# Performance work log

Hardware: AMD Instinct MI355X
Metric: run time of the kernel (lower is better)

Reference implementation:

```python
import jax, jax.numpy as jnp
import numpy as np

B, N, M = 8, 1024, 1024
DIM2 = 1280          # config.dim * 2
KIN = 1344           # esm_dim + cell_line_dim
H, DK = 8, 64        # heads, attn_dim_key
SCALE = DK ** -0.5


def setup_inputs() -> dict:
    key = jax.random.key(0)
    ks = jax.random.split(key, 7)
    rna_reps = jax.random.normal(ks[0], (B, N, DIM2), dtype=jnp.float32)
    protein_reps = jax.random.normal(ks[1], (B, M, KIN), dtype=jnp.float32)
    # learned params (Linear stores weight [out, in])
    Wq = jax.random.normal(ks[2], (H * DK, DIM2), dtype=jnp.float32) * (DIM2 ** -0.5)
    bq = jnp.zeros((H * DK,), dtype=jnp.float32)
    Wk = jax.random.normal(ks[3], (H * DK, KIN), dtype=jnp.float32) * (KIN ** -0.5)
    bk = jnp.zeros((H * DK,), dtype=jnp.float32)
    rel_bias = jax.random.normal(ks[4], (1, H, 1, DK), dtype=jnp.float32)
    return {"rna_reps": rna_reps, "protein_reps": protein_reps,
            "Wq": Wq, "bq": bq, "Wk": Wk, "bk": bk, "rel_bias": rel_bias}


def reference(rna_reps, protein_reps, Wq, bq, Wk, bk, rel_bias):
    b = rna_reps.shape[0]
    q = rna_reps @ Wq.T + bq           # [b, n, h*dk]
    k = protein_reps @ Wk.T + bk       # [b, m, h*dk]
    q = q.reshape(b, N, H, DK).transpose(0, 2, 1, 3)   # b h n d
    k = k.reshape(b, M, H, DK).transpose(0, 2, 1, 3)   # b h m d
    q = q * SCALE
    logits = jnp.einsum('bhid,bhjd->bhij', q + rel_bias, k)  # [b,h,n,m]
    out = jnp.mean(logits, axis=1)     # mean over heads -> [b,n,m]
    # dropout p=0.0 (eval) -> identity
    return out
```

## Files before the change

### kernel.cpp

```cpp
#include <hip/hip_runtime.h>
#include <hip/hip_bf16.h>


typedef __bf16 bf16x8 __attribute__((ext_vector_type(8)));
typedef float f32x4 __attribute__((ext_vector_type(4)));

__device__ inline bf16x8 cvt2(const f32x4 a, const f32x4 b) {
    bf16x8 r;
    r[0] = (__bf16)a[0]; r[1] = (__bf16)a[1]; r[2] = (__bf16)a[2]; r[3] = (__bf16)a[3];
    r[4] = (__bf16)b[0]; r[5] = (__bf16)b[1]; r[6] = (__bf16)b[2]; r[7] = (__bf16)b[3];
    return r;
}

#define GLDS(src, dst) __builtin_amdgcn_global_load_lds( \
    (const __attribute__((address_space(1))) void*)(src), \
    (__attribute__((address_space(3))) void*)(dst), 16, 0, 0)

__global__ __launch_bounds__(256)
void wcvt(const float* __restrict__ Wq, const float* __restrict__ Wk,
          __bf16* __restrict__ wqb, __bf16* __restrict__ wkb)
{
    const int id = blockIdx.x * 256 + threadIdx.x;
    const int NQ = 512 * 160;
    const float* src; __bf16* dst; int row, p, K;
    if (id < NQ) { row = id / 160; p = id - row * 160; K = 1280; src = Wq; dst = wqb; }
    else { const int t = id - NQ; row = t / 168; p = t - row * 168; K = 1344; src = Wk; dst = wkb; }
    const int m3 = ((row & 3) << 1) | ((row >> 2) & 1);
    const int c  = (p & ~7) | ((p & 7) ^ m3);
    const f32x4 v0 = *(const f32x4*)(src + (size_t)row * K + c * 8);
    const f32x4 v1 = *(const f32x4*)(src + (size_t)row * K + c * 8 + 4);
    *(bf16x8*)(dst + (size_t)row * K + p * 8) = cvt2(v0, v1);
}

__global__ __launch_bounds__(512, 4)
void proj_all(const float* __restrict__ rna,  const float* __restrict__ prot,
              const __bf16* __restrict__ wqb, const __bf16* __restrict__ wkb,
              const float* __restrict__ bq,   const float* __restrict__ bk,
              const float* __restrict__ rb,
              __bf16* __restrict__ qout, __bf16* __restrict__ kout)
{
    __shared__ float  As[64 * 64];
    __shared__ __bf16 Ws[256 * 64];

    const int bid = blockIdx.x;
    const int wg  = (bid & 7) * 64 + (bid >> 3);
    const bool isQ = wg < 256;
    const int lwg  = isQ ? wg : wg - 256;
    const int brow = (lwg >> 1) * 64;
    const int bcol = (lwg & 1) * 256;

    const float*  A    = isQ ? rna : prot;
    const __bf16* Wb   = isQ ? wqb : wkb;
    const float*  bias = isQ ? bq  : bk;
    __bf16*       out  = isQ ? qout : kout;
    const int     K    = isQ ? 1280 : 1344;

    const int tid  = threadIdx.x;
    const int lane = tid & 63;
    const int wid  = tid >> 6;
    const int fr   = lane & 15;
    const int q4   = lane >> 4;

    const int lrow = lane >> 4;
    const int ciA  = (lane & 15) ^ (lrow << 1);
    const float* aG0 = A + (size_t)(brow + wid * 8 + 0 + lrow) * K + ciA * 4;
    const float* aG1 = A + (size_t)(brow + wid * 8 + 4 + lrow) * K + (ciA ^ 1) * 4;

    const __bf16* wG = Wb + (size_t)(bcol + wid * 32 + (lane >> 3)) * K + (lane & 7) * 8;

    const int rmask = ((fr & 3) << 1) | ((fr >> 2) & 1);

    f32x4 acc[4][2] = {};

    for (int k0 = 0; k0 < K; k0 += 64) {
        __syncthreads();
        GLDS(aG0 + k0, &As[wid * 512]);
        GLDS(aG1 + k0, &As[wid * 512 + 256]);
        #pragma unroll
        for (int j = 0; j < 4; ++j)
            GLDS(wG + (size_t)(j * 8) * K + k0, &Ws[(wid * 32 + j * 8) * 64]);
        __syncthreads();

        #pragma unroll
        for (int kk = 0; kk < 2; ++kk) {
            const int c0 = kk * 8 + 2 * q4;
            const int cw = kk * 4 + q4;
            bf16x8 af[4], bw[2];
            #pragma unroll
            for (int m = 0; m < 4; ++m) {
                const float* rp = &As[(m * 16 + fr) * 64];
                f32x4 u0 = *(const f32x4*)(rp + (((c0    ) ^ rmask) << 2));
                f32x4 u1 = *(const f32x4*)(rp + (((c0 + 1) ^ rmask) << 2));
                af[m] = cvt2(u0, u1);
            }
            #pragma unroll
            for (int n = 0; n < 2; ++n)
                bw[n] = *(const bf16x8*)(&Ws[(wid * 32 + n * 16 + fr) * 64
                                             + ((cw ^ rmask) << 3)]);
            #pragma unroll
            for (int m = 0; m < 4; ++m)
                #pragma unroll
                for (int n = 0; n < 2; ++n)
                    acc[m][n] = __builtin_amdgcn_mfma_f32_16x16x32_bf16(af[m], bw[n], acc[m][n], 0, 0, 0);
        }
    }

    const int r0 = q4 * 4;
    #pragma unroll
    for (int n = 0; n < 2; ++n) {
        const int c = bcol + wid * 32 + n * 16 + fr;
        const float bv = bias[c];
        const float rv = isQ ? rb[c] : 0.0f;
        #pragma unroll
        for (int m = 0; m < 4; ++m) {
            const int row = brow + m * 16 + r0;
            #pragma unroll
            for (int j = 0; j < 4; ++j) {
                float v = acc[m][n][j] + bv;
                if (isQ) v = 0.125f * v + rv;
                out[(size_t)(row + j) * 512 + c] = (__bf16)v;
            }
        }
    }
}

__global__ __launch_bounds__(256, 2)
void attn_kernel(const __bf16* __restrict__ Q,
                 const __bf16* __restrict__ Kb,
                 float* __restrict__ out)
{
    __shared__ __bf16 As[128 * 64];
    __shared__ __bf16 Bs[128 * 64];

    const int tid  = threadIdx.x;
    const int lane = tid & 63;
    const int wid  = tid >> 6;
    const int wr   = wid >> 1;
    const int wc   = wid & 1;
    const int b    = blockIdx.z;
    const int brow = blockIdx.y * 128;
    const int bcol = blockIdx.x * 128;

    const __bf16* Qb = Q  + (size_t)b * 1024 * 512;
    const __bf16* Kp = Kb + (size_t)b * 1024 * 512;

    const int fr = lane & 15;
    const int q4 = lane >> 4;

    f32x4 acc[4][4] = {};

    const int lr3 = lane >> 3;
    const int m3  = ((lr3 & 3) << 1) | ((lr3 >> 2) & 1);
    const int scol = ((lane & 7) ^ m3) * 8;
    const int rmask = ((fr & 3) << 1) | ((fr >> 2) & 1);

    for (int k0 = 0; k0 < 512; k0 += 64) {
        __syncthreads();
        #pragma unroll
        for (int i = 0; i < 4; ++i) {
            const int rbase = wid * 32 + i * 8;
            GLDS(Qb + (size_t)(brow + rbase + lr3) * 512 + k0 + scol, &As[rbase * 64]);
            GLDS(Kp + (size_t)(bcol + rbase + lr3) * 512 + k0 + scol, &Bs[rbase * 64]);
        }
        __syncthreads();

        #pragma unroll
        for (int kk = 0; kk < 2; ++kk) {
            const int ci = kk * 4 + q4;
            bf16x8 af[4], bf_[4];
            #pragma unroll
            for (int m = 0; m < 4; ++m)
                af[m] = *(const bf16x8*)(&As[(wr * 64 + m * 16 + fr) * 64 + ((ci ^ rmask) << 3)]);
            #pragma unroll
            for (int n = 0; n < 4; ++n)
                bf_[n] = *(const bf16x8*)(&Bs[(wc * 64 + n * 16 + fr) * 64 + ((ci ^ rmask) << 3)]);
            #pragma unroll
            for (int m = 0; m < 4; ++m)
                #pragma unroll
                for (int n = 0; n < 4; ++n)
                    acc[m][n] = __builtin_amdgcn_mfma_f32_16x16x32_bf16(af[m], bf_[n], acc[m][n], 0, 0, 0);
        }
    }

    float* op = out + (size_t)b * 1024 * 1024;
    const int r0 = (lane >> 4) * 4;
    #pragma unroll
    for (int n = 0; n < 4; ++n) {
        const int col = bcol + wc * 64 + n * 16 + fr;
        #pragma unroll
        for (int m = 0; m < 4; ++m) {
            const int row = brow + wr * 64 + m * 16 + r0;
            #pragma unroll
            for (int j = 0; j < 4; ++j)
                op[(size_t)(row + j) * 1024 + col] = 0.125f * acc[m][n][j];
        }
    }
}

extern "C" void kernel_launch(void* const* d_in, const int* in_sizes, int n_in,
                              void* d_out, int out_size, void* d_ws, size_t ws_size,
                              hipStream_t stream) {
    const float* rna  = (const float*)d_in[0];
    const float* prot = (const float*)d_in[1];
    const float* Wq   = (const float*)d_in[2];
    const float* bq   = (const float*)d_in[3];
    const float* Wk   = (const float*)d_in[4];
    const float* bk   = (const float*)d_in[5];
    const float* rb   = (const float*)d_in[6];

    __bf16* qws = (__bf16*)d_ws;
    __bf16* kws = qws + (size_t)8192 * 512;
    __bf16* wqb = kws + (size_t)8192 * 512;
    __bf16* wkb = wqb + (size_t)512 * 1280;

    wcvt<<<dim3(656), dim3(256), 0, stream>>>(Wq, Wk, wqb, wkb);
    proj_all<<<dim3(512), dim3(512), 0, stream>>>(rna, prot, wqb, wkb, bq, bk, rb, qws, kws);
    attn_kernel<<<dim3(8, 8, 8), dim3(256), 0, stream>>>(qws, kws, (float*)d_out);
}
```

Before: 63.67 us.

## Enlarge projection GEMM tile to 128x256 per block with 2x2 warp grid

The projection kernel now computes a 128-row by 256-column tile per block using 4 waves in a 2x2 arrangement, each holding a 64x128 accumulator, instead of 64x256 tiles over 8 waves. This raises arithmetic intensity per LDS load and halves redundant weight traffic across blocks. The trade-off is that only 256 blocks of 256 threads launch (one per CU on mi355x), with far more registers per thread and lower occupancy for hiding latency. The fp32 A-tile swizzle is changed to a 4-bit mask to match the new layout.

```diff
diff --git a/kernel.cpp b/kernel.cpp
--- a/kernel.cpp
+++ b/kernel.cpp
@@ -32,21 +32,21 @@
     *(bf16x8*)(dst + (size_t)row * K + p * 8) = cvt2(v0, v1);
 }
 
-__global__ __launch_bounds__(512, 4)
+__global__ __launch_bounds__(256, 1)
 void proj_all(const float* __restrict__ rna,  const float* __restrict__ prot,
               const __bf16* __restrict__ wqb, const __bf16* __restrict__ wkb,
               const float* __restrict__ bq,   const float* __restrict__ bk,
               const float* __restrict__ rb,
               __bf16* __restrict__ qout, __bf16* __restrict__ kout)
 {
-    __shared__ float  As[64 * 64];
+    __shared__ float  As[128 * 64];
     __shared__ __bf16 Ws[256 * 64];
 
     const int bid = blockIdx.x;
-    const int wg  = (bid & 7) * 64 + (bid >> 3);
-    const bool isQ = wg < 256;
-    const int lwg  = isQ ? wg : wg - 256;
-    const int brow = (lwg >> 1) * 64;
+    const int wg  = (bid & 7) * 32 + (bid >> 3);
+    const bool isQ = wg < 128;
+    const int lwg  = isQ ? wg : wg - 128;
+    const int brow = (lwg >> 1) * 128;
     const int bcol = (lwg & 1) * 256;
 
     const float*  A    = isQ ? rna : prot;
@@ -58,62 +58,71 @@
     const int tid  = threadIdx.x;
     const int lane = tid & 63;
     const int wid  = tid >> 6;
+    const int wr   = wid >> 1;
+    const int wc   = wid & 1;
     const int fr   = lane & 15;
     const int q4   = lane >> 4;
 
     const int lrow = lane >> 4;
-    const int ciA  = (lane & 15) ^ (lrow << 1);
-    const float* aG0 = A + (size_t)(brow + wid * 8 + 0 + lrow) * K + ciA * 4;
-    const float* aG1 = A + (size_t)(brow + wid * 8 + 4 + lrow) * K + (ciA ^ 1) * 4;
-
-    const __bf16* wG = Wb + (size_t)(bcol + wid * 32 + (lane >> 3)) * K + (lane & 7) * 8;
-
-    const int rmask = ((fr & 3) << 1) | ((fr >> 2) & 1);
-
-    f32x4 acc[4][2] = {};
+    const float* aB[4];
+    #pragma unroll
+    for (int j = 0; j < 4; ++j) {
+        const int ci = (lane & 15) ^ ((lrow << 2) | j);
+        aB[j] = A + (size_t)(brow + wid * 32 + j * 4 + lrow) * K + ci * 4;
+    }
+
+    const __bf16* wG = Wb + (size_t)(bcol + wid * 64 + (lane >> 3)) * K + (lane & 7) * 8;
+
+    const int rmask4 = ((fr & 3) << 2) | (fr >> 2);
+    const int rmask3 = ((fr & 3) << 1) | ((fr >> 2) & 1);
+
+    f32x4 acc[4][8] = {};
 
     for (int k0 = 0; k0 < K; k0 += 64) {
         __syncthreads();
-        GLDS(aG0 + k0, &As[wid * 512]);
-        GLDS(aG1 + k0, &As[wid * 512 + 256]);
-        #pragma unroll
-        for (int j = 0; j < 4; ++j)
-            GLDS(wG + (size_t)(j * 8) * K + k0, &Ws[(wid * 32 + j * 8) * 64]);
+        #pragma unroll
+        for (int i = 0; i < 8; ++i)
+            GLDS(aB[i & 3] + (size_t)((i >> 2) * 16) * K + k0,
+                 &As[(wid * 32 + i * 4) * 64]);
+        #pragma unroll
+        for (int j = 0; j < 8; ++j)
+            GLDS(wG + (size_t)(j * 8) * K + k0,
+                 &Ws[(wid * 64 + j * 8) * 64]);
         __syncthreads();
 
         #pragma unroll
         for (int kk = 0; kk < 2; ++kk) {
-            const int c0 = kk * 8 + 2 * q4;
+            const int g0 = kk * 8 + 2 * q4;
             const int cw = kk * 4 + q4;
-            bf16x8 af[4], bw[2];
+            bf16x8 af[4], bw[8];
             #pragma unroll
             for (int m = 0; m < 4; ++m) {
-                const float* rp = &As[(m * 16 + fr) * 64];
-                f32x4 u0 = *(const f32x4*)(rp + (((c0    ) ^ rmask) << 2));
-                f32x4 u1 = *(const f32x4*)(rp + (((c0 + 1) ^ rmask) << 2));
+                const float* rp = &As[(wr * 64 + m * 16 + fr) * 64];
+                f32x4 u0 = *(const f32x4*)(rp + (((g0    ) ^ rmask4) << 2));
+                f32x4 u1 = *(const f32x4*)(rp + (((g0 + 1) ^ rmask4) << 2));
                 af[m] = cvt2(u0, u1);
             }
             #pragma unroll
-            for (int n = 0; n < 2; ++n)
-                bw[n] = *(const bf16x8*)(&Ws[(wid * 32 + n * 16 + fr) * 64
-                                             + ((cw ^ rmask) << 3)]);
+            for (int n = 0; n < 8; ++n)
+                bw[n] = *(const bf16x8*)(&Ws[(wc * 128 + n * 16 + fr) * 64
+                                             + ((cw ^ rmask3) << 3)]);
             #pragma unroll
             for (int m = 0; m < 4; ++m)
                 #pragma unroll
-                for (int n = 0; n < 2; ++n)
+                for (int n = 0; n < 8; ++n)
                     acc[m][n] = __builtin_amdgcn_mfma_f32_16x16x32_bf16(af[m], bw[n], acc[m][n], 0, 0, 0);
         }
     }
 
     const int r0 = q4 * 4;
     #pragma unroll
-    for (int n = 0; n < 2; ++n) {
-        const int c = bcol + wid * 32 + n * 16 + fr;
+    for (int n = 0; n < 8; ++n) {
+        const int c = bcol + wc * 128 + n * 16 + fr;
         const float bv = bias[c];
         const float rv = isQ ? rb[c] : 0.0f;
         #pragma unroll
         for (int m = 0; m < 4; ++m) {
-            const int row = brow + m * 16 + r0;
+            const int row = brow + wr * 64 + m * 16 + r0;
             #pragma unroll
             for (int j = 0; j < 4; ++j) {
                 float v = acc[m][n][j] + bv;
@@ -214,6 +223,6 @@
     __bf16* wkb = wqb + (size_t)512 * 1280;
 
     wcvt<<<dim3(656), dim3(256), 0, stream>>>(Wq, Wk, wqb, wkb);
-    proj_all<<<dim3(512), dim3(512), 0, stream>>>(rna, prot, wqb, wkb, bq, bk, rb, qws, kws);
+    proj_all<<<dim3(256), dim3(256), 0, stream>>>(rna, prot, wqb, wkb, bq, bk, rb, qws, kws);
     attn_kernel<<<dim3(8, 8, 8), dim3(256), 0, stream>>>(qws, kws, (float*)d_out);
 }
```

Result: slower. 74.28 us (+16.7%).
